# Performance work log

Measured on AMD Instinct MI355X. Metric: run time of the kernel, lower is better.

Reference implementation:

```python
import jax, jax.numpy as jnp
import numpy as np

B, T, C = 2, 2048, 1024
NH = 16
HD = C // NH


def setup_inputs() -> dict:
    key = jax.random.key(0)
    k1, k2, k3 = jax.random.split(key, 3)
    x = jax.random.normal(k1, (B, T, C), dtype=jnp.float32)
    w_qkv = jax.random.normal(k2, (C, 3 * C), dtype=jnp.float32) * (C ** -0.5)
    w_proj = jax.random.normal(k3, (C, C), dtype=jnp.float32) * (C ** -0.5)
    return {"x": x, "w_qkv": w_qkv, "w_proj": w_proj}


def reference(x, w_qkv, w_proj):
    Bv, Tv, Cv = x.shape
    qkv = x @ w_qkv  # [B, T, 3C]
    q, k, v = jnp.split(qkv, 3, axis=-1)
    # [B, T, C] -> [B, NH, T, HD]
    q = q.reshape(Bv, Tv, NH, HD).transpose(0, 2, 1, 3)
    k = k.reshape(Bv, Tv, NH, HD).transpose(0, 2, 1, 3)
    v = v.reshape(Bv, Tv, NH, HD).transpose(0, 2, 1, 3)
    att = jnp.einsum("bhqd,bhkd->bhqk", q, k) * (HD ** -0.5)
    causal = jnp.tril(jnp.ones((Tv, Tv), dtype=bool))  # [T, T]
    att = jnp.where(causal[None, None, :, :], att, -jnp.inf)
    att = jax.nn.softmax(att, axis=-1)
    # dropout p=0.0 (eval) -> identity
    y = jnp.einsum("bhqk,bhkd->bhqd", att, v)  # [B, NH, T, HD]
    y = y.transpose(0, 2, 1, 3).reshape(Bv, Tv, Cv)
    return y @ w_proj
```

## Files before the change

### kernel.cpp

```cpp
#include <hip/hip_runtime.h>
#include <hip/hip_bf16.h>

#define B_ 2
#define T_ 2048
#define C_ 1024
#define NH_ 16
#define HD_ 64

using bf16 = __hip_bfloat16;
typedef __attribute__((ext_vector_type(8))) short bf16x8;
typedef __attribute__((ext_vector_type(4))) float f32x4;

__device__ __forceinline__ float bf2f(unsigned short u) {
    union { unsigned int i; float f; } v;
    v.i = ((unsigned int)u) << 16;
    return v.f;
}
__device__ __forceinline__ unsigned short f2bf(float f) {
    union { float f; unsigned int u; } v;
    v.f = f;
    unsigned int r = v.u + 0x7fffu + ((v.u >> 16) & 1u);
    return (unsigned short)(r >> 16);
}
__device__ __forceinline__ unsigned int cvt_pk_bf16(float lo, float hi) {
    unsigned int r;
    asm("v_cvt_pk_bf16_f32 %0, %1, %2" : "=v"(r) : "v"(lo), "v"(hi));
    return r;
}
__device__ __forceinline__ void gld_lds16(const void* g, void* l) {
    __builtin_amdgcn_global_load_lds(
        (__attribute__((address_space(1))) void*)g,
        (__attribute__((address_space(3))) void*)l, 16, 0, 0);
}

__global__ __launch_bounds__(256) void prep(
    const float* __restrict__ X, const float* __restrict__ Wq,
    unsigned short* __restrict__ Xb, unsigned short* __restrict__ Wqt) {
    __shared__ short S[64][72];
    const int b = blockIdx.x;
    const int t = threadIdx.x;
    if (b < 2048) {
        int i = (b * 256 + t) * 8;
        float4 f0 = *reinterpret_cast<const float4*>(&X[i]);
        float4 f1 = *reinterpret_cast<const float4*>(&X[i + 4]);
        union { unsigned short s[8]; uint4 v; } o;
        o.s[0] = f2bf(f0.x); o.s[1] = f2bf(f0.y); o.s[2] = f2bf(f0.z); o.s[3] = f2bf(f0.w);
        o.s[4] = f2bf(f1.x); o.s[5] = f2bf(f1.y); o.s[6] = f2bf(f1.z); o.s[7] = f2bf(f1.w);
        *reinterpret_cast<uint4*>(&Xb[i]) = o.v;
        return;
    }
    const int idx = b - 2048;
    const int n0 = (idx % 48) * 64, k0 = (idx / 48) * 64;
    const int NN = 3 * C_, KK = C_;
    const int lr = t >> 2, lc = (t & 3) * 16;
    const float* src = &Wq[(size_t)(k0 + lr) * NN + n0 + lc];
    #pragma unroll
    for (int j4 = 0; j4 < 4; ++j4) {
        float4 f = *reinterpret_cast<const float4*>(src + j4 * 4);
        S[lc + j4 * 4 + 0][lr] = (short)f2bf(f.x);
        S[lc + j4 * 4 + 1][lr] = (short)f2bf(f.y);
        S[lc + j4 * 4 + 2][lr] = (short)f2bf(f.z);
        S[lc + j4 * 4 + 3][lr] = (short)f2bf(f.w);
    }
    __syncthreads();
    union { unsigned short s[16]; uint4 v[2]; } o;
    #pragma unroll
    for (int j = 0; j < 16; ++j) o.s[j] = (unsigned short)S[lr][lc + j];
    unsigned short* dst = &Wqt[(size_t)(n0 + lr) * KK + k0 + lc];
    *reinterpret_cast<uint4*>(dst)     = o.v[0];
    *reinterpret_cast<uint4*>(dst + 8) = o.v[1];
}

__global__ __launch_bounds__(256) void post(
    const unsigned short* __restrict__ V, unsigned short* __restrict__ Vt,
    const float* __restrict__ Wp, unsigned short* __restrict__ Wpt) {
    __shared__ short S[64][72];
    const int b = blockIdx.x;
    const int t = threadIdx.x;
    const int lr = t >> 2, lc = (t & 3) * 16;
    if (b < 1024) {
        const int bh = b >> 5, t0 = (b & 31) * 64;
        const unsigned short* src = V + ((size_t)bh * T_ + t0 + lr) * HD_ + lc;
        union { uint4 v[2]; unsigned short s[16]; } u;
        u.v[0] = *reinterpret_cast<const uint4*>(src);
        u.v[1] = *reinterpret_cast<const uint4*>(src + 8);
        #pragma unroll
        for (int j = 0; j < 16; ++j) S[lc + j][lr] = (short)u.s[j];
        __syncthreads();
        union { unsigned short s[16]; uint4 v[2]; } o;
        #pragma unroll
        for (int j = 0; j < 16; ++j) o.s[j] = (unsigned short)S[lr][lc + j];
        unsigned short* dst = Vt + ((size_t)bh * HD_ + lr) * T_ + t0 + lc;
        *reinterpret_cast<uint4*>(dst)     = o.v[0];
        *reinterpret_cast<uint4*>(dst + 8) = o.v[1];
        return;
    }
    const int idx = b - 1024;
    const int n0 = (idx & 15) * 64, k0 = (idx >> 4) * 64;
    const float* src = &Wp[(size_t)(k0 + lr) * C_ + n0 + lc];
    #pragma unroll
    for (int j4 = 0; j4 < 4; ++j4) {
        float4 f = *reinterpret_cast<const float4*>(src + j4 * 4);
        S[lc + j4 * 4 + 0][lr] = (short)f2bf(f.x);
        S[lc + j4 * 4 + 1][lr] = (short)f2bf(f.y);
        S[lc + j4 * 4 + 2][lr] = (short)f2bf(f.z);
        S[lc + j4 * 4 + 3][lr] = (short)f2bf(f.w);
    }
    __syncthreads();
    union { unsigned short s[16]; uint4 v[2]; } o;
    #pragma unroll
    for (int j = 0; j < 16; ++j) o.s[j] = (unsigned short)S[lr][lc + j];
    unsigned short* dst = &Wpt[(size_t)(n0 + lr) * C_ + k0 + lc];
    *reinterpret_cast<uint4*>(dst)     = o.v[0];
    *reinterpret_cast<uint4*>(dst + 8) = o.v[1];
}

__global__ __launch_bounds__(256) void qkv_gemm_mfma(
    const unsigned short* __restrict__ A, const unsigned short* __restrict__ Bt,
    unsigned short* __restrict__ Qb, unsigned short* __restrict__ Kb,
    unsigned short* __restrict__ Vb) {
    __shared__ short As[2][128 * 32];
    __shared__ short Bs[2][128 * 32];
    const int t = threadIdx.x;
    const int wid = t >> 6, lane = t & 63;
    const int wm = wid >> 1, wn = wid & 1;
    const int c = lane & 15, g = lane >> 4;
    const int dd = blockIdx.x;
    const int w  = (dd & 7) * 96 + (dd >> 3);
    const int m0 = (w / 24) * 128, n0 = (w % 24) * 128;
    const int K = C_;
    const int srow = t >> 2, skk = (t & 3) * 8;

    f32x4 acc[4][4];
    #pragma unroll
    for (int i = 0; i < 4; ++i)
        #pragma unroll
        for (int j = 0; j < 4; ++j) acc[i][j] = (f32x4){0.f, 0.f, 0.f, 0.f};

    gld_lds16(&A[(size_t)(m0 + srow) * K + skk],       As[0] + t * 8);
    gld_lds16(&A[(size_t)(m0 + 64 + srow) * K + skk],  As[0] + 2048 + t * 8);
    gld_lds16(&Bt[(size_t)(n0 + srow) * K + skk],      Bs[0] + t * 8);
    gld_lds16(&Bt[(size_t)(n0 + 64 + srow) * K + skk], Bs[0] + 2048 + t * 8);

    #pragma unroll 1
    for (int kt = 0; kt < 32; ++kt) {
        const int cur = kt & 1;
        __syncthreads();
        if (kt < 31) {
            const int k0 = (kt + 1) * 32;
            gld_lds16(&A[(size_t)(m0 + srow) * K + k0 + skk],       As[cur ^ 1] + t * 8);
            gld_lds16(&A[(size_t)(m0 + 64 + srow) * K + k0 + skk],  As[cur ^ 1] + 2048 + t * 8);
            gld_lds16(&Bt[(size_t)(n0 + srow) * K + k0 + skk],      Bs[cur ^ 1] + t * 8);
            gld_lds16(&Bt[(size_t)(n0 + 64 + srow) * K + k0 + skk], Bs[cur ^ 1] + 2048 + t * 8);
        }
        bf16x8 af[4], bfv[4];
        #pragma unroll
        for (int mi = 0; mi < 4; ++mi)
            af[mi] = *reinterpret_cast<const bf16x8*>(&As[cur][(wm * 64 + mi * 16 + c) * 32 + g * 8]);
        #pragma unroll
        for (int ni = 0; ni < 4; ++ni)
            bfv[ni] = *reinterpret_cast<const bf16x8*>(&Bs[cur][(wn * 64 + ni * 16 + c) * 32 + g * 8]);
        #pragma unroll
        for (int mi = 0; mi < 4; ++mi)
            #pragma unroll
            for (int ni = 0; ni < 4; ++ni)
                acc[mi][ni] = __builtin_amdgcn_mfma_f32_16x16x32_bf16(af[mi], bfv[ni], acc[mi][ni], 0, 0, 0);
    }

    const int nbase = n0 + wn * 64;
    const int which = nbase >> 10;
    const int h     = (nbase >> 6) & (NH_ - 1);
    const float scale = (which == 0) ? 0.125f * 1.44269504f : 1.0f;
    unsigned short* dst = (which == 0) ? Qb : ((which == 1) ? Kb : Vb);
    #pragma unroll
    for (int mi = 0; mi < 4; ++mi)
        #pragma unroll
        for (int r = 0; r < 4; ++r) {
            const int m = m0 + wm * 64 + mi * 16 + 4 * g + r;
            const int bb = m >> 11, tq = m & (T_ - 1);
            unsigned short* p = dst + ((size_t)((bb << 4) | h) * T_ + tq) * HD_;
            #pragma unroll
            for (int ni = 0; ni < 4; ++ni)
                p[ni * 16 + c] = f2bf(acc[mi][ni][r] * scale);
        }
}

__global__ __launch_bounds__(256) void proj_gemm_mfma(
    const unsigned short* __restrict__ A, const unsigned short* __restrict__ Bt,
    float* __restrict__ Out) {
    __shared__ short As[2][64 * 32];
    __shared__ short Bs[2][128 * 32];
    const int t = threadIdx.x;
    const int wid = t >> 6, lane = t & 63;
    const int wm = wid >> 1, wn = wid & 1;
    const int c = lane & 15, g = lane >> 4;
    const int m0 = blockIdx.y * 64, n0 = blockIdx.x * 128;
    const int K = C_;
    const int srow = t >> 2, skk = (t & 3) * 8;

    f32x4 acc[2][4];
    #pragma unroll
    for (int i = 0; i < 2; ++i)
        #pragma unroll
        for (int j = 0; j < 4; ++j) acc[i][j] = (f32x4){0.f, 0.f, 0.f, 0.f};

    gld_lds16(&A[(size_t)(m0 + srow) * K + skk],       As[0] + t * 8);
    gld_lds16(&Bt[(size_t)(n0 + srow) * K + skk],      Bs[0] + t * 8);
    gld_lds16(&Bt[(size_t)(n0 + 64 + srow) * K + skk], Bs[0] + 2048 + t * 8);

    #pragma unroll 1
    for (int kt = 0; kt < 32; ++kt) {
        const int cur = kt & 1;
        __syncthreads();
        if (kt < 31) {
            const int k0 = (kt + 1) * 32;
            gld_lds16(&A[(size_t)(m0 + srow) * K + k0 + skk],       As[cur ^ 1] + t * 8);
            gld_lds16(&Bt[(size_t)(n0 + srow) * K + k0 + skk],      Bs[cur ^ 1] + t * 8);
            gld_lds16(&Bt[(size_t)(n0 + 64 + srow) * K + k0 + skk], Bs[cur ^ 1] + 2048 + t * 8);
        }
        bf16x8 af[2], bfv[4];
        #pragma unroll
        for (int mi = 0; mi < 2; ++mi)
            af[mi] = *reinterpret_cast<const bf16x8*>(&As[cur][(wm * 32 + mi * 16 + c) * 32 + g * 8]);
        #pragma unroll
        for (int ni = 0; ni < 4; ++ni)
            bfv[ni] = *reinterpret_cast<const bf16x8*>(&Bs[cur][(wn * 64 + ni * 16 + c) * 32 + g * 8]);
        #pragma unroll
        for (int mi = 0; mi < 2; ++mi)
            #pragma unroll
            for (int ni = 0; ni < 4; ++ni)
                acc[mi][ni] = __builtin_amdgcn_mfma_f32_16x16x32_bf16(af[mi], bfv[ni], acc[mi][ni], 0, 0, 0);
    }

    #pragma unroll
    for (int mi = 0; mi < 2; ++mi)
        #pragma unroll
        for (int r = 0; r < 4; ++r) {
            const int m = m0 + wm * 32 + mi * 16 + 4 * g + r;
            float* p = Out + (size_t)m * C_ + n0 + wn * 64;
            #pragma unroll
            for (int ni = 0; ni < 4; ++ni)
                p[ni * 16 + c] = acc[mi][ni][r];
        }
}

__global__ __launch_bounds__(512) void attn_mfma(
    const unsigned short* __restrict__ Qb, const unsigned short* __restrict__ Kb,
    const unsigned short* __restrict__ Vt_g, unsigned short* __restrict__ Yu) {
    __shared__ short Ks[2][64][72];
    __shared__ short Vt[2][64][72];

    const int t    = threadIdx.x;
    const int wid  = t >> 6;
    const int lane = t & 63;
    const int c    = lane & 15;
    const int g    = lane >> 4;

    const int d   = blockIdx.x;
    const int xcd = d & 7;
    const int tt  = d >> 3;
    const int up  = tt & 15;
    const int k2  = tt >> 4;
    const int bh  = (k2 << 3) | xcd;
    const int u   = (k2 & 2) ? (15 - up) : up;
    const int qtB = 2 * u + 1;
    const int myqt = (wid < 4) ? (2 * u) : qtB;

    const int bb = bh >> 4, h = bh & (NH_ - 1);
    const int qw0 = (wid & 3) * 16;
    const int q0  = myqt * 64;

    const unsigned short* Qh  = Qb   + (size_t)bh * T_ * HD_;
    const unsigned short* Kh  = Kb   + (size_t)bh * T_ * HD_;
    const unsigned short* VTh = Vt_g + (size_t)bh * HD_ * T_;

    const int srow = t >> 3, scol = (t & 7) * 8;
    const int jA = scol, jB = scol + 4;
    const int slotA = 32 * (jA >> 5) + 8 * ((jA >> 2) & 3) + 4 * ((jA >> 4) & 1);
    const int slotB = 32 * (jB >> 5) + 8 * ((jB >> 2) & 3) + 4 * ((jB >> 4) & 1);

    bf16x8 qf0, qf1;
    {
        const unsigned short* qs = Qh + (size_t)(q0 + qw0 + c) * HD_ + g * 8;
        qf0 = *reinterpret_cast<const bf16x8*>(qs);
        qf1 = *reinterpret_cast<const bf16x8*>(qs + 32);
    }

    float l_run = 0.f;
    f32x4 yacc[4];
    #pragma unroll
    for (int nt = 0; nt < 4; ++nt) yacc[nt] = (f32x4){0.f, 0.f, 0.f, 0.f};

    uint4 kv, vv;
    {
        kv = *reinterpret_cast<const uint4*>(&Kh[(size_t)srow * HD_ + scol]);
        vv = *reinterpret_cast<const uint4*>(&VTh[(size_t)srow * T_ + scol]);
    }

    #pragma unroll 1
    for (int kt = 0; kt <= qtB; ++kt) {
        const int cur = kt & 1;
        *reinterpret_cast<uint4*>(&Ks[cur][srow][scol]) = kv;
        *reinterpret_cast<uint2*>(&Vt[cur][srow][slotA]) = make_uint2(vv.x, vv.y);
        *reinterpret_cast<uint2*>(&Vt[cur][srow][slotB]) = make_uint2(vv.z, vv.w);
        __syncthreads();

        if (kt < qtB) {
            const int j1 = (kt + 1) * 64;
            kv = *reinterpret_cast<const uint4*>(&Kh[(size_t)(j1 + srow) * HD_ + scol]);
            vv = *reinterpret_cast<const uint4*>(&VTh[(size_t)srow * T_ + j1 + scol]);
        }

        if (kt <= myqt) {
            f32x4 sacc[4];
            #pragma unroll
            for (int nt = 0; nt < 4; ++nt) sacc[nt] = (f32x4){0.f, 0.f, 0.f, 0.f};
            __builtin_amdgcn_s_setprio(1);
            #pragma unroll
            for (int kk = 0; kk < 2; ++kk) {
                const bf16x8 qf = kk ? qf1 : qf0;
                #pragma unroll
                for (int nt = 0; nt < 4; ++nt) {
                    bf16x8 kf = *reinterpret_cast<const bf16x8*>(&Ks[cur][nt * 16 + c][kk * 32 + g * 8]);
                    sacc[nt] = __builtin_amdgcn_mfma_f32_16x16x32_bf16(kf, qf, sacc[nt], 0, 0, 0);
                }
            }
            __builtin_amdgcn_s_setprio(0);

            const bool diag = (kt == myqt);
            float p[4][4];
            float lsum = 0.f;
            #pragma unroll
            for (int nt = 0; nt < 4; ++nt)
                #pragma unroll
                for (int r = 0; r < 4; ++r) {
                    float s = sacc[nt][r];
                    if (diag && (nt * 16 + 4 * g + r > qw0 + c)) s = -1e30f;
                    float pv = exp2f(s);
                    p[nt][r] = pv;
                    lsum += pv;
                }
            l_run += lsum;

            unsigned int pk[8];
            #pragma unroll
            for (int nt = 0; nt < 4; ++nt) {
                pk[2 * nt]     = cvt_pk_bf16(p[nt][0], p[nt][1]);
                pk[2 * nt + 1] = cvt_pk_bf16(p[nt][2], p[nt][3]);
            }

            __builtin_amdgcn_s_setprio(1);
            #pragma unroll
            for (int kk = 0; kk < 2; ++kk) {
                union { unsigned int w[4]; bf16x8 v; } pa;
                pa.w[0] = pk[4 * kk + 0]; pa.w[1] = pk[4 * kk + 1];
                pa.w[2] = pk[4 * kk + 2]; pa.w[3] = pk[4 * kk + 3];
                #pragma unroll
                for (int nt = 0; nt < 4; ++nt) {
                    bf16x8 vb = *reinterpret_cast<const bf16x8*>(&Vt[cur][nt * 16 + c][kk * 32 + g * 8]);
                    yacc[nt] = __builtin_amdgcn_mfma_f32_16x16x32_bf16(pa.v, vb, yacc[nt], 0, 0, 0);
                }
            }
            __builtin_amdgcn_s_setprio(0);
        }
    }

    float lf = l_run;
    lf += __shfl_xor(lf, 16, 64);
    lf += __shfl_xor(lf, 32, 64);
    const float inv = 1.0f / lf;
    const int ii = __float_as_int(inv);
    float invr[4];
    #pragma unroll
    for (int r = 0; r < 4; ++r)
        invr[r] = __int_as_float(__builtin_amdgcn_ds_bpermute((4 * g + r) * 4, ii));
    #pragma unroll
    for (int r = 0; r < 4; ++r) {
        const size_t row = (size_t)(bb * T_ + q0 + qw0 + 4 * g + r);
        #pragma unroll
        for (int nt = 0; nt < 4; ++nt) {
            const int col = h * HD_ + 16 * nt + c;
            Yu[row * C_ + col] = f2bf(yacc[nt][r] * invr[r]);
        }
    }
}

extern "C" void kernel_launch(void* const* d_in, const int* in_sizes, int n_in,
                              void* d_out, int out_size, void* d_ws, size_t ws_size,
                              hipStream_t stream) {
    const float* x      = (const float*)d_in[0];
    const float* w_qkv  = (const float*)d_in[1];
    const float* w_proj = (const float*)d_in[2];
    float* out = (float*)d_out;

    const size_t HELEMS = (size_t)B_ * NH_ * T_ * HD_;
    unsigned short* Qb   = (unsigned short*)d_ws;
    unsigned short* Kb   = Qb + HELEMS;
    unsigned short* Vraw = Kb + HELEMS;
    unsigned short* Yb   = Vraw;
    unsigned short* Xb   = Vraw + HELEMS;
    unsigned short* Vt   = Xb;
    unsigned short* Wqt  = Xb + HELEMS;
    unsigned short* Wpt  = Wqt;

    prep<<<2816, 256, 0, stream>>>(x, w_qkv, Xb, Wqt);
    qkv_gemm_mfma<<<768, 256, 0, stream>>>(Xb, Wqt, Qb, Kb, Vraw);
    post<<<1280, 256, 0, stream>>>(Vraw, Vt, w_proj, Wpt);
    attn_mfma<<<512, 512, 0, stream>>>(Qb, Kb, Vt, Yb);
    proj_gemm_mfma<<<dim3(8, 64), 256, 0, stream>>>(Yb, Wpt, out);
}
```

Measured before the change: 113.6 us.

## Switch attention to 32x32x16 MFMA tiles with 4 waves per block

Rewrites the attention kernel to use 32x32x16 bf16 MFMA instructions instead of 16x16x32. Each wave now handles 32 query rows, and the block shrinks from 512 to 256 threads (4 waves), with launch bounds requesting 2 blocks per CU. K/V staging loads double per thread and the V LDS swizzle is recomputed for the new fragment layout. The row-sum reduction and output store become simpler: a single cross-half shuffle and packed 8-byte bf16 writes. The cost is more accumulator registers per wave and less wave-level parallelism per block.

Result: slower. 128.3 us (+12.9%).

```diff
diff --git a/kernel.cpp b/kernel.cpp
--- a/kernel.cpp
+++ b/kernel.cpp
@@ -10,6 +10,7 @@
 using bf16 = __hip_bfloat16;
 typedef __attribute__((ext_vector_type(8))) short bf16x8;
 typedef __attribute__((ext_vector_type(4))) float f32x4;
+typedef __attribute__((ext_vector_type(16))) float f32x16;
 
 __device__ __forceinline__ float bf2f(unsigned short u) {
     union { unsigned int i; float f; } v;
@@ -244,7 +245,7 @@
         }
 }
 
-__global__ __launch_bounds__(512) void attn_mfma(
+__global__ __launch_bounds__(256, 2) void attn_mfma(
     const unsigned short* __restrict__ Qb, const unsigned short* __restrict__ Kb,
     const unsigned short* __restrict__ Vt_g, unsigned short* __restrict__ Yu) {
     __shared__ short Ks[2][64][72];
@@ -253,8 +254,8 @@
     const int t    = threadIdx.x;
     const int wid  = t >> 6;
     const int lane = t & 63;
-    const int c    = lane & 15;
-    const int g    = lane >> 4;
+    const int ql   = lane & 31;
+    const int h    = lane >> 5;
 
     const int d   = blockIdx.x;
     const int xcd = d & 7;
@@ -264,101 +265,114 @@
     const int bh  = (k2 << 3) | xcd;
     const int u   = (k2 & 2) ? (15 - up) : up;
     const int qtB = 2 * u + 1;
-    const int myqt = (wid < 4) ? (2 * u) : qtB;
-
-    const int bb = bh >> 4, h = bh & (NH_ - 1);
-    const int qw0 = (wid & 3) * 16;
-    const int q0  = myqt * 64;
+    const int myqt = (wid < 2) ? (2 * u) : qtB;
+
+    const int bb = bh >> 4, hh = bh & (NH_ - 1);
+    const int qglob = myqt * 64 + (wid & 1) * 32 + ql;
 
     const unsigned short* Qh  = Qb   + (size_t)bh * T_ * HD_;
     const unsigned short* Kh  = Kb   + (size_t)bh * T_ * HD_;
     const unsigned short* VTh = Vt_g + (size_t)bh * HD_ * T_;
 
-    const int srow = t >> 3, scol = (t & 7) * 8;
-    const int jA = scol, jB = scol + 4;
-    const int slotA = 32 * (jA >> 5) + 8 * ((jA >> 2) & 3) + 4 * ((jA >> 4) & 1);
-    const int slotB = 32 * (jB >> 5) + 8 * ((jB >> 2) & 3) + 4 * ((jB >> 4) & 1);
-
-    bf16x8 qf0, qf1;
+    const int srow = t >> 2, scol = (t & 3) * 16;
+    int kap[4];
+    #pragma unroll
+    for (int m = 0; m < 4; ++m) {
+        const int j = scol + 4 * m;
+        kap[m] = ((j >> 3) & 3) * 16 + ((j >> 2) & 1) * 8 + (j >> 5) * 4;
+    }
+
+    bf16x8 qf[4];
     {
-        const unsigned short* qs = Qh + (size_t)(q0 + qw0 + c) * HD_ + g * 8;
-        qf0 = *reinterpret_cast<const bf16x8*>(qs);
-        qf1 = *reinterpret_cast<const bf16x8*>(qs + 32);
+        const unsigned short* qs = Qh + (size_t)qglob * HD_ + 8 * h;
+        #pragma unroll
+        for (int s = 0; s < 4; ++s)
+            qf[s] = *reinterpret_cast<const bf16x8*>(qs + s * 16);
     }
 
     float l_run = 0.f;
-    f32x4 yacc[4];
-    #pragma unroll
-    for (int nt = 0; nt < 4; ++nt) yacc[nt] = (f32x4){0.f, 0.f, 0.f, 0.f};
-
-    uint4 kv, vv;
+    f32x16 yacc[2];
+    yacc[0] = (f32x16)(0.f);
+    yacc[1] = (f32x16)(0.f);
+
+    uint4 kv0, kv1, vv0, vv1;
     {
-        kv = *reinterpret_cast<const uint4*>(&Kh[(size_t)srow * HD_ + scol]);
-        vv = *reinterpret_cast<const uint4*>(&VTh[(size_t)srow * T_ + scol]);
+        const unsigned short* ks = &Kh[(size_t)srow * HD_ + scol];
+        kv0 = *reinterpret_cast<const uint4*>(ks);
+        kv1 = *reinterpret_cast<const uint4*>(ks + 8);
+        const unsigned short* vs = &VTh[(size_t)srow * T_ + scol];
+        vv0 = *reinterpret_cast<const uint4*>(vs);
+        vv1 = *reinterpret_cast<const uint4*>(vs + 8);
     }
 
     #pragma unroll 1
     for (int kt = 0; kt <= qtB; ++kt) {
         const int cur = kt & 1;
-        *reinterpret_cast<uint4*>(&Ks[cur][srow][scol]) = kv;
-        *reinterpret_cast<uint2*>(&Vt[cur][srow][slotA]) = make_uint2(vv.x, vv.y);
-        *reinterpret_cast<uint2*>(&Vt[cur][srow][slotB]) = make_uint2(vv.z, vv.w);
+        *reinterpret_cast<uint4*>(&Ks[cur][srow][scol])     = kv0;
+        *reinterpret_cast<uint4*>(&Ks[cur][srow][scol + 8]) = kv1;
+        *reinterpret_cast<uint2*>(&Vt[cur][srow][kap[0]]) = make_uint2(vv0.x, vv0.y);
+        *reinterpret_cast<uint2*>(&Vt[cur][srow][kap[1]]) = make_uint2(vv0.z, vv0.w);
+        *reinterpret_cast<uint2*>(&Vt[cur][srow][kap[2]]) = make_uint2(vv1.x, vv1.y);
+        *reinterpret_cast<uint2*>(&Vt[cur][srow][kap[3]]) = make_uint2(vv1.z, vv1.w);
         __syncthreads();
 
         if (kt < qtB) {
             const int j1 = (kt + 1) * 64;
-            kv = *reinterpret_cast<const uint4*>(&Kh[(size_t)(j1 + srow) * HD_ + scol]);
-            vv = *reinterpret_cast<const uint4*>(&VTh[(size_t)srow * T_ + j1 + scol]);
+            const unsigned short* ks = &Kh[(size_t)(j1 + srow) * HD_ + scol];
+            kv0 = *reinterpret_cast<const uint4*>(ks);
+            kv1 = *reinterpret_cast<const uint4*>(ks + 8);
+            const unsigned short* vs = &VTh[(size_t)srow * T_ + j1 + scol];
+            vv0 = *reinterpret_cast<const uint4*>(vs);
+            vv1 = *reinterpret_cast<const uint4*>(vs + 8);
         }
 
         if (kt <= myqt) {
-            f32x4 sacc[4];
-            #pragma unroll
-            for (int nt = 0; nt < 4; ++nt) sacc[nt] = (f32x4){0.f, 0.f, 0.f, 0.f};
+            f32x16 sacc[2];
+            sacc[0] = (f32x16)(0.f);
+            sacc[1] = (f32x16)(0.f);
             __builtin_amdgcn_s_setprio(1);
             #pragma unroll
-            for (int kk = 0; kk < 2; ++kk) {
-                const bf16x8 qf = kk ? qf1 : qf0;
+            for (int s = 0; s < 4; ++s) {
                 #pragma unroll
-                for (int nt = 0; nt < 4; ++nt) {
-                    bf16x8 kf = *reinterpret_cast<const bf16x8*>(&Ks[cur][nt * 16 + c][kk * 32 + g * 8]);
-                    sacc[nt] = __builtin_amdgcn_mfma_f32_16x16x32_bf16(kf, qf, sacc[nt], 0, 0, 0);
+                for (int nt = 0; nt < 2; ++nt) {
+                    bf16x8 kf = *reinterpret_cast<const bf16x8*>(
+                        &Ks[cur][nt * 32 + ql][s * 16 + 8 * h]);
+                    sacc[nt] = __builtin_amdgcn_mfma_f32_32x32x16_bf16(kf, qf[s], sacc[nt], 0, 0, 0);
                 }
             }
             __builtin_amdgcn_s_setprio(0);
 
             const bool diag = (kt == myqt);
-            float p[4][4];
+            float p[2][16];
             float lsum = 0.f;
             #pragma unroll
-            for (int nt = 0; nt < 4; ++nt)
+            for (int nt = 0; nt < 2; ++nt)
                 #pragma unroll
-                for (int r = 0; r < 4; ++r) {
+                for (int r = 0; r < 16; ++r) {
                     float s = sacc[nt][r];
-                    if (diag && (nt * 16 + 4 * g + r > qw0 + c)) s = -1e30f;
+                    if (diag) {
+                        const int jg = kt * 64 + nt * 32 + (r & 3) + 8 * (r >> 2) + 4 * h;
+                        if (jg > qglob) s = -1e30f;
+                    }
                     float pv = exp2f(s);
                     p[nt][r] = pv;
                     lsum += pv;
                 }
             l_run += lsum;
 
-            unsigned int pk[8];
-            #pragma unroll
-            for (int nt = 0; nt < 4; ++nt) {
-                pk[2 * nt]     = cvt_pk_bf16(p[nt][0], p[nt][1]);
-                pk[2 * nt + 1] = cvt_pk_bf16(p[nt][2], p[nt][3]);
-            }
-
             __builtin_amdgcn_s_setprio(1);
             #pragma unroll
-            for (int kk = 0; kk < 2; ++kk) {
-                union { unsigned int w[4]; bf16x8 v; } pa;
-                pa.w[0] = pk[4 * kk + 0]; pa.w[1] = pk[4 * kk + 1];
-                pa.w[2] = pk[4 * kk + 2]; pa.w[3] = pk[4 * kk + 3];
+            for (int s = 0; s < 4; ++s) {
+                union { unsigned int w[4]; bf16x8 v; } pb;
+                pb.w[0] = cvt_pk_bf16(p[0][4 * s + 0], p[0][4 * s + 1]);
+                pb.w[1] = cvt_pk_bf16(p[0][4 * s + 2], p[0][4 * s + 3]);
+                pb.w[2] = cvt_pk_bf16(p[1][4 * s + 0], p[1][4 * s + 1]);
+                pb.w[3] = cvt_pk_bf16(p[1][4 * s + 2], p[1][4 * s + 3]);
                 #pragma unroll
-                for (int nt = 0; nt < 4; ++nt) {
-                    bf16x8 vb = *reinterpret_cast<const bf16x8*>(&Vt[cur][nt * 16 + c][kk * 32 + g * 8]);
-                    yacc[nt] = __builtin_amdgcn_mfma_f32_16x16x32_bf16(pa.v, vb, yacc[nt], 0, 0, 0);
+                for (int dt = 0; dt < 2; ++dt) {
+                    bf16x8 vf = *reinterpret_cast<const bf16x8*>(
+                        &Vt[cur][dt * 32 + ql][s * 16 + 8 * h]);
+                    yacc[dt] = __builtin_amdgcn_mfma_f32_32x32x16_bf16(vf, pb.v, yacc[dt], 0, 0, 0);
                 }
             }
             __builtin_amdgcn_s_setprio(0);
@@ -366,23 +380,18 @@
     }
 
     float lf = l_run;
-    lf += __shfl_xor(lf, 16, 64);
     lf += __shfl_xor(lf, 32, 64);
     const float inv = 1.0f / lf;
-    const int ii = __float_as_int(inv);
-    float invr[4];
-    #pragma unroll
-    for (int r = 0; r < 4; ++r)
-        invr[r] = __int_as_float(__builtin_amdgcn_ds_bpermute((4 * g + r) * 4, ii));
-    #pragma unroll
-    for (int r = 0; r < 4; ++r) {
-        const size_t row = (size_t)(bb * T_ + q0 + qw0 + 4 * g + r);
-        #pragma unroll
-        for (int nt = 0; nt < 4; ++nt) {
-            const int col = h * HD_ + 16 * nt + c;
-            Yu[row * C_ + col] = f2bf(yacc[nt][r] * invr[r]);
-        }
-    }
+    unsigned short* base = &Yu[(size_t)(bb * T_ + qglob) * C_ + hh * HD_];
+    #pragma unroll
+    for (int dt = 0; dt < 2; ++dt)
+        #pragma unroll
+        for (int b4 = 0; b4 < 4; ++b4) {
+            uint2 ow;
+            ow.x = cvt_pk_bf16(yacc[dt][4 * b4 + 0] * inv, yacc[dt][4 * b4 + 1] * inv);
+            ow.y = cvt_pk_bf16(yacc[dt][4 * b4 + 2] * inv, yacc[dt][4 * b4 + 3] * inv);
+            *reinterpret_cast<uint2*>(base + dt * 32 + 8 * b4 + 4 * h) = ow;
+        }
 }
 
 extern "C" void kernel_launch(void* const* d_in, const int* in_sizes, int n_in,
@@ -406,6 +415,6 @@
     prep<<<2816, 256, 0, stream>>>(x, w_qkv, Xb, Wqt);
     qkv_gemm_mfma<<<768, 256, 0, stream>>>(Xb, Wqt, Qb, Kb, Vraw);
     post<<<1280, 256, 0, stream>>>(Vraw, Vt, w_proj, Wpt);
-    attn_mfma<<<512, 512, 0, stream>>>(Qb, Kb, Vt, Yb);
+    attn_mfma<<<512, 256, 0, stream>>>(Qb, Kb, Vt, Yb);
     proj_gemm_mfma<<<dim3(8, 64), 256, 0, stream>>>(Yb, Wpt, out);
 }
```
